# Optimization experiments

Hardware: AMD Instinct MI355X
Metric: run time of the kernel (lower is better)

The kernel has to match this reference:

```python
import jax, jax.numpy as jnp
import numpy as np

BS, H, S, DK = 4, 16, 1024, 64  # bs, n_heads, seq_len(=q_len), head_dim


def setup_inputs() -> dict:
    key = jax.random.key(0)
    k1, k2, k3, k4 = jax.random.split(key, 4)
    return {
        "q": jax.random.normal(k1, (BS, H, S, DK), dtype=jnp.float32),
        "k": jax.random.normal(k2, (BS, H, DK, S), dtype=jnp.float32),
        "v": jax.random.normal(k3, (BS, H, S, DK), dtype=jnp.float32),
        "prev": jax.random.normal(k4, (BS, H, S, S), dtype=jnp.float32),
        "attn_mask": jnp.zeros((1, S, S), dtype=jnp.float32),  # additive float mask
        "key_padding_mask": jnp.zeros((BS, S), dtype=bool),     # True = masked key
        "scale": jnp.asarray(DK ** -0.5, dtype=jnp.float32),    # learnable (lsa=True)
    }


def reference(q, k, v, prev, attn_mask, key_padding_mask, scale):
    # attn_scores = q @ k * scale + prev + attn_mask (float branch)
    scores = jnp.einsum("bhqd,bhdk->bhqk", q, k) * scale
    scores = scores + prev + attn_mask[:, None, :, :]  # [1,S,S] -> broadcast over b,h
    # key_padding_mask: [bs, seq_len] -> masked_fill(-inf)
    scores = jnp.where(key_padding_mask[:, None, None, :], -jnp.inf, scores)
    attn = jax.nn.softmax(scores, axis=-1)  # dropout p=0.0 -> identity
    out = jnp.einsum("bhqk,bhkd->bhqd", attn, v)
    # res_attention=True -> (output, attn_weights, attn_scores)
    return out, attn, scores
```

## Files before the change

### kernel.cpp

```cpp
#include <hip/hip_runtime.h>
#include <math.h>

#define SEQ 1024
#define DKH 64
#define QBLK 64
#define NTILE 16
#define KSTR 68

typedef short s8v __attribute__((ext_vector_type(8)));
typedef short s4v __attribute__((ext_vector_type(4)));
typedef float f4v __attribute__((ext_vector_type(4)));

__device__ __forceinline__ short f2bf(float f) {
    unsigned u = __builtin_bit_cast(unsigned, f);
    return (short)((u + 0x8000u) >> 16);
}
__device__ __forceinline__ s8v ld_frag(const unsigned short* p) {
    s4v a = *(const s4v*)(p);
    s4v b = *(const s4v*)(p + 4);
    s8v r;
    r[0]=a[0]; r[1]=a[1]; r[2]=a[2]; r[3]=a[3];
    r[4]=b[0]; r[5]=b[1]; r[6]=b[2]; r[7]=b[3];
    return r;
}

__global__ __launch_bounds__(256, 3)
void qk_scores(const float* __restrict__ q, const float* __restrict__ k,
               const float* __restrict__ prev, const float* __restrict__ mask,
               const unsigned char* __restrict__ kpm, const float* __restrict__ scale_p,
               float* __restrict__ scores, float* __restrict__ inv_ws)
{
    __shared__ unsigned short q_s[QBLK * KSTR];
    __shared__ unsigned short k_s[64 * KSTR];

    const int t   = threadIdx.x;
    const int w   = t >> 6;
    const int l   = t & 63;
    const int g   = l >> 4;
    const int c16 = l & 15;
    const int sa  = t & 15, sg = t >> 4;

    const int wg  = blockIdx.x;
    const int swz = (wg & 7) * 128 + (wg >> 3);
    const int bh  = swz >> 4;
    const int rt  = swz & 15;
    const int b   = bh >> 4;

    const float scale = *scale_p;

    const float* qb = q    + ((size_t)bh * SEQ + rt * QBLK) * DKH;
    const float* kb = k    + (size_t)bh * DKH * SEQ;
    const float* pb = prev + ((size_t)bh * SEQ + rt * QBLK) * SEQ;
    const float* mb = mask + (size_t)(rt * QBLK) * SEQ;
    const unsigned char* kp = kpm + (size_t)b * SEQ;
    float* sb = scores + ((size_t)bh * SEQ + rt * QBLK) * SEQ;

    {
        const int row = t >> 2, c0 = (t & 3) * 16;
        const float* src = qb + row * DKH + c0;
        #pragma unroll
        for (int j = 0; j < 4; ++j) {
            f4v f = *(const f4v*)(src + 4 * j);
            s4v h; h[0]=f2bf(f[0]); h[1]=f2bf(f[1]); h[2]=f2bf(f[2]); h[3]=f2bf(f[3]);
            *(s4v*)&q_s[row * KSTR + c0 + 4 * j] = h;
        }
    }
    __syncthreads();
    const s8v aq0 = ld_frag(&q_s[(w * 16 + c16) * KSTR + g * 8]);
    const s8v aq1 = ld_frag(&q_s[(w * 16 + c16) * KSTR + 32 + g * 8]);

    f4v kreg[4];
    auto load_K = [&](int ct) {
        const float* src = kb + (size_t)(4 * sg) * SEQ + ct * 64 + 4 * sa;
        kreg[0] = *(const f4v*)(src);
        kreg[1] = *(const f4v*)(src + SEQ);
        kreg[2] = *(const f4v*)(src + 2 * SEQ);
        kreg[3] = *(const f4v*)(src + 3 * SEQ);
    };
    auto load_PM = [&](int ct, float (&pr)[16], float (&mr)[16], int (&kf)[4]) {
        #pragma unroll
        for (int r = 0; r < 4; ++r) {
            const float* prow = pb + (size_t)(w * 16 + 4 * g + r) * SEQ + ct * 64 + c16;
            const float* mrow = mb + (size_t)(w * 16 + 4 * g + r) * SEQ + ct * 64 + c16;
            #pragma unroll
            for (int s = 0; s < 4; ++s) {
                pr[r * 4 + s] = __builtin_nontemporal_load(prow + s * 16);
                mr[r * 4 + s] = mrow[s * 16];
            }
        }
        #pragma unroll
        for (int s = 0; s < 4; ++s) kf[s] = kp[ct * 64 + s * 16 + c16];
    };

    float l_r[4] = {0.f, 0.f, 0.f, 0.f};
    float prA[16], mrA[16], prB[16], mrB[16];
    int kfA[4], kfB[4];
    load_K(0);
    load_PM(0, prA, mrA, kfA);

    auto tile = [&](int ct, float (&prc)[16], float (&mrc)[16], int (&kfc)[4],
                    float (&prn)[16], float (&mrn)[16], int (&kfn)[4]) {
        __syncthreads();
        #pragma unroll
        for (int j = 0; j < 4; ++j) {
            s4v hk; hk[0]=f2bf(kreg[0][j]); hk[1]=f2bf(kreg[1][j]); hk[2]=f2bf(kreg[2][j]); hk[3]=f2bf(kreg[3][j]);
            *(s4v*)&k_s[(4 * sa + j) * KSTR + 4 * sg] = hk;
        }
        __syncthreads();

        if (ct + 1 < NTILE) load_K(ct + 1);

        f4v acc[4];
        #pragma unroll
        for (int s = 0; s < 4; ++s) acc[s] = 0;
        #pragma unroll
        for (int s = 0; s < 4; ++s) {
            const s8v bk0 = ld_frag(&k_s[(s * 16 + c16) * KSTR + g * 8]);
            acc[s] = __builtin_amdgcn_mfma_f32_16x16x32_bf16(aq0, bk0, acc[s], 0, 0, 0);
            const s8v bk1 = ld_frag(&k_s[(s * 16 + c16) * KSTR + 32 + g * 8]);
            acc[s] = __builtin_amdgcn_mfma_f32_16x16x32_bf16(aq1, bk1, acc[s], 0, 0, 0);
        }

        if (ct + 1 < NTILE) load_PM(ct + 1, prn, mrn, kfn);

        const int colb = ct * 64;
        #pragma unroll
        for (int r = 0; r < 4; ++r) {
            float* srow = sb + (size_t)(w * 16 + 4 * g + r) * SEQ + colb + c16;
            #pragma unroll
            for (int s = 0; s < 4; ++s) {
                float x = fmaf(acc[s][r], scale, prc[r * 4 + s] + mrc[r * 4 + s]);
                x = kfc[s] ? -INFINITY : x;
                srow[s * 16] = x;
                l_r[r] += __expf(x);
            }
        }
    };

    for (int c2 = 0; c2 < NTILE; c2 += 2) {
        tile(c2,     prA, mrA, kfA, prB, mrB, kfB);
        tile(c2 + 1, prB, mrB, kfB, prA, mrA, kfA);
    }

    #pragma unroll
    for (int off = 1; off <= 8; off <<= 1) {
        #pragma unroll
        for (int r = 0; r < 4; ++r) l_r[r] += __shfl_xor(l_r[r], off, 64);
    }
    if (c16 == 0) {
        #pragma unroll
        for (int r = 0; r < 4; ++r)
            inv_ws[(size_t)bh * SEQ + rt * QBLK + w * 16 + 4 * g + r] = 1.0f / l_r[r];
    }
}

__global__ __launch_bounds__(256, 3)
void pv_attn(const float* __restrict__ v, const float* __restrict__ scores,
             const float* __restrict__ inv_ws,
             float* __restrict__ attn, float* __restrict__ out)
{
    __shared__ unsigned short v_s[64 * KSTR];
    __shared__ unsigned short e_s[4][16 * KSTR];

    const int t   = threadIdx.x;
    const int w   = t >> 6;
    const int l   = t & 63;
    const int g   = l >> 4;
    const int c16 = l & 15;
    const int sa  = t & 15, sg = t >> 4;

    const int wg  = blockIdx.x;
    const int swz = (wg & 7) * 128 + (wg >> 3);
    const int bh  = swz >> 4;
    const int rt  = swz & 15;

    const float* vb  = v      + (size_t)bh * SEQ * DKH;
    const float* sbr = scores + ((size_t)bh * SEQ + rt * QBLK) * SEQ;
    float* ab = attn + ((size_t)bh * SEQ + rt * QBLK) * SEQ;
    float* ob = out  + ((size_t)bh * SEQ + rt * QBLK) * DKH;

    float inv_r[4];
    #pragma unroll
    for (int r = 0; r < 4; ++r)
        inv_r[r] = inv_ws[(size_t)bh * SEQ + rt * QBLK + w * 16 + g * 4 + r];

    f4v vreg[4];
    auto load_V = [&](int ct) {
        const float* src = vb + (size_t)(ct * 64 + 4 * sg) * DKH + 4 * sa;
        vreg[0] = *(const f4v*)(src);
        vreg[1] = *(const f4v*)(src + DKH);
        vreg[2] = *(const f4v*)(src + 2 * DKH);
        vreg[3] = *(const f4v*)(src + 3 * DKH);
    };
    auto load_S = [&](int ct, f4v (&sr)[4]) {
        #pragma unroll
        for (int r = 0; r < 4; ++r)
            sr[r] = *(const f4v*)(sbr + (size_t)(w * 16 + g * 4 + r) * SEQ + ct * 64 + c16 * 4);
    };

    f4v oacc[4];
    #pragma unroll
    for (int d = 0; d < 4; ++d) oacc[d] = 0;

    f4v sregA[4], sregB[4];
    load_V(0);
    load_S(0, sregA);

    auto tile = [&](int ct, f4v (&sc)[4], f4v (&sn)[4]) {
        __syncthreads();
        #pragma unroll
        for (int j = 0; j < 4; ++j) {
            s4v hv; hv[0]=f2bf(vreg[0][j]); hv[1]=f2bf(vreg[1][j]); hv[2]=f2bf(vreg[2][j]); hv[3]=f2bf(vreg[3][j]);
            *(s4v*)&v_s[(4 * sa + j) * KSTR + 4 * sg] = hv;
        }
        __syncthreads();

        if (ct + 1 < NTILE) { load_V(ct + 1); load_S(ct + 1, sn); }

        #pragma unroll
        for (int r = 0; r < 4; ++r) {
            const f4v s4 = sc[r];
            const float e0 = __expf(s4[0]);
            const float e1 = __expf(s4[1]);
            const float e2 = __expf(s4[2]);
            const float e3 = __expf(s4[3]);
            f4v aw; aw[0]=e0*inv_r[r]; aw[1]=e1*inv_r[r]; aw[2]=e2*inv_r[r]; aw[3]=e3*inv_r[r];
            __builtin_nontemporal_store(aw,
                (f4v*)(ab + (size_t)(w * 16 + g * 4 + r) * SEQ + ct * 64 + c16 * 4));
            s4v h; h[0]=f2bf(e0); h[1]=f2bf(e1); h[2]=f2bf(e2); h[3]=f2bf(e3);
            *(s4v*)&e_s[w][(g * 4 + r) * KSTR + c16 * 4] = h;
        }

        #pragma unroll
        for (int ks = 0; ks < 2; ++ks) {
            const s8v ae = ld_frag(&e_s[w][c16 * KSTR + ks * 32 + g * 8]);
            #pragma unroll
            for (int d = 0; d < 4; ++d) {
                const s8v bv = ld_frag(&v_s[(d * 16 + c16) * KSTR + ks * 32 + g * 8]);
                oacc[d] = __builtin_amdgcn_mfma_f32_16x16x32_bf16(ae, bv, oacc[d], 0, 0, 0);
            }
        }
    };

    for (int c2 = 0; c2 < NTILE; c2 += 2) {
        tile(c2,     sregA, sregB);
        tile(c2 + 1, sregB, sregA);
    }

    #pragma unroll
    for (int d = 0; d < 4; ++d) {
        #pragma unroll
        for (int r = 0; r < 4; ++r)
            __builtin_nontemporal_store(oacc[d][r] * inv_r[r],
                ob + (size_t)(w * 16 + g * 4 + r) * DKH + d * 16 + c16);
    }
}

extern "C" void kernel_launch(void* const* d_in, const int* in_sizes, int n_in,
                              void* d_out, int out_size, void* d_ws, size_t ws_size,
                              hipStream_t stream) {
    const float* q    = (const float*)d_in[0];
    const float* k    = (const float*)d_in[1];
    const float* v    = (const float*)d_in[2];
    const float* prev = (const float*)d_in[3];
    const float* mask = (const float*)d_in[4];
    const unsigned char* kpm = (const unsigned char*)d_in[5];
    const float* scale = (const float*)d_in[6];

    float* out    = (float*)d_out;
    float* attn   = out  + (size_t)4 * 16 * SEQ * DKH;
    float* scores = attn + (size_t)4 * 16 * SEQ * SEQ;
    float* inv_ws = (float*)d_ws;

    qk_scores<<<dim3(1024), dim3(256), 0, stream>>>(q, k, prev, mask, kpm, scale,
                                                    scores, inv_ws);
    pv_attn<<<dim3(1024), dim3(256), 0, stream>>>(v, scores, inv_ws, attn, out);
}
```

Before: 276.9 us.

## Fuse score and PV kernels into one kernel re-reading scores within block

```diff
diff --git a/kernel.cpp b/kernel.cpp
--- a/kernel.cpp
+++ b/kernel.cpp
@@ -24,14 +24,18 @@
     return r;
 }
 
-__global__ __launch_bounds__(256, 3)
-void qk_scores(const float* __restrict__ q, const float* __restrict__ k,
-               const float* __restrict__ prev, const float* __restrict__ mask,
-               const unsigned char* __restrict__ kpm, const float* __restrict__ scale_p,
-               float* __restrict__ scores, float* __restrict__ inv_ws)
+__global__ __launch_bounds__(256, 4)
+void attn_fused(const float* __restrict__ q, const float* __restrict__ k,
+                const float* __restrict__ v, const float* __restrict__ prev,
+                const float* __restrict__ mask, const unsigned char* __restrict__ kpm,
+                const float* __restrict__ scale_p,
+                float* __restrict__ out, float* __restrict__ attn,
+                float* __restrict__ scores)
 {
     __shared__ unsigned short q_s[QBLK * KSTR];
-    __shared__ unsigned short k_s[64 * KSTR];
+    __shared__ unsigned short kv_s[64 * KSTR];
+    __shared__ unsigned short e_s[4][16 * KSTR];
+    __shared__ float inv_sh[QBLK];
 
     const int t   = threadIdx.x;
     const int w   = t >> 6;
@@ -50,10 +54,13 @@
 
     const float* qb = q    + ((size_t)bh * SEQ + rt * QBLK) * DKH;
     const float* kb = k    + (size_t)bh * DKH * SEQ;
+    const float* vb = v    + (size_t)bh * SEQ * DKH;
     const float* pb = prev + ((size_t)bh * SEQ + rt * QBLK) * SEQ;
     const float* mb = mask + (size_t)(rt * QBLK) * SEQ;
     const unsigned char* kp = kpm + (size_t)b * SEQ;
     float* sb = scores + ((size_t)bh * SEQ + rt * QBLK) * SEQ;
+    float* ab = attn   + ((size_t)bh * SEQ + rt * QBLK) * SEQ;
+    float* ob = out    + ((size_t)bh * SEQ + rt * QBLK) * DKH;
 
     {
         const int row = t >> 2, c0 = (t & 3) * 16;
@@ -77,34 +84,28 @@
         kreg[2] = *(const f4v*)(src + 2 * SEQ);
         kreg[3] = *(const f4v*)(src + 3 * SEQ);
     };
-    auto load_PM = [&](int ct, float (&pr)[16], float (&mr)[16], int (&kf)[4]) {
+    auto load_PM = [&](int ct, float (&pm)[16]) {
         #pragma unroll
         for (int r = 0; r < 4; ++r) {
             const float* prow = pb + (size_t)(w * 16 + 4 * g + r) * SEQ + ct * 64 + c16;
             const float* mrow = mb + (size_t)(w * 16 + 4 * g + r) * SEQ + ct * 64 + c16;
             #pragma unroll
-            for (int s = 0; s < 4; ++s) {
-                pr[r * 4 + s] = __builtin_nontemporal_load(prow + s * 16);
-                mr[r * 4 + s] = mrow[s * 16];
-            }
-        }
-        #pragma unroll
-        for (int s = 0; s < 4; ++s) kf[s] = kp[ct * 64 + s * 16 + c16];
+            for (int s = 0; s < 4; ++s)
+                pm[r * 4 + s] = __builtin_nontemporal_load(prow + s * 16) + mrow[s * 16];
+        }
     };
 
     float l_r[4] = {0.f, 0.f, 0.f, 0.f};
-    float prA[16], mrA[16], prB[16], mrB[16];
-    int kfA[4], kfB[4];
+    float pmA[16], pmB[16];
     load_K(0);
-    load_PM(0, prA, mrA, kfA);
-
-    auto tile = [&](int ct, float (&prc)[16], float (&mrc)[16], int (&kfc)[4],
-                    float (&prn)[16], float (&mrn)[16], int (&kfn)[4]) {
+    load_PM(0, pmA);
+
+    auto tile1 = [&](int ct, float (&pmc)[16], float (&pmn)[16]) {
         __syncthreads();
         #pragma unroll
         for (int j = 0; j < 4; ++j) {
             s4v hk; hk[0]=f2bf(kreg[0][j]); hk[1]=f2bf(kreg[1][j]); hk[2]=f2bf(kreg[2][j]); hk[3]=f2bf(kreg[3][j]);
-            *(s4v*)&k_s[(4 * sa + j) * KSTR + 4 * sg] = hk;
+            *(s4v*)&kv_s[(4 * sa + j) * KSTR + 4 * sg] = hk;
         }
         __syncthreads();
 
@@ -115,22 +116,25 @@
         for (int s = 0; s < 4; ++s) acc[s] = 0;
         #pragma unroll
         for (int s = 0; s < 4; ++s) {
-            const s8v bk0 = ld_frag(&k_s[(s * 16 + c16) * KSTR + g * 8]);
+            const s8v bk0 = ld_frag(&kv_s[(s * 16 + c16) * KSTR + g * 8]);
             acc[s] = __builtin_amdgcn_mfma_f32_16x16x32_bf16(aq0, bk0, acc[s], 0, 0, 0);
-            const s8v bk1 = ld_frag(&k_s[(s * 16 + c16) * KSTR + 32 + g * 8]);
+            const s8v bk1 = ld_frag(&kv_s[(s * 16 + c16) * KSTR + 32 + g * 8]);
             acc[s] = __builtin_amdgcn_mfma_f32_16x16x32_bf16(aq1, bk1, acc[s], 0, 0, 0);
         }
 
-        if (ct + 1 < NTILE) load_PM(ct + 1, prn, mrn, kfn);
+        if (ct + 1 < NTILE) load_PM(ct + 1, pmn);
 
         const int colb = ct * 64;
+        int kf[4];
+        #pragma unroll
+        for (int s = 0; s < 4; ++s) kf[s] = kp[colb + s * 16 + c16];
         #pragma unroll
         for (int r = 0; r < 4; ++r) {
             float* srow = sb + (size_t)(w * 16 + 4 * g + r) * SEQ + colb + c16;
             #pragma unroll
             for (int s = 0; s < 4; ++s) {
-                float x = fmaf(acc[s][r], scale, prc[r * 4 + s] + mrc[r * 4 + s]);
-                x = kfc[s] ? -INFINITY : x;
+                float x = fmaf(acc[s][r], scale, pmc[r * 4 + s]);
+                x = kf[s] ? -INFINITY : x;
                 srow[s * 16] = x;
                 l_r[r] += __expf(x);
             }
@@ -138,8 +142,8 @@
     };
 
     for (int c2 = 0; c2 < NTILE; c2 += 2) {
-        tile(c2,     prA, mrA, kfA, prB, mrB, kfB);
-        tile(c2 + 1, prB, mrB, kfB, prA, mrA, kfA);
+        tile1(c2,     pmA, pmB);
+        tile1(c2 + 1, pmB, pmA);
     }
 
     #pragma unroll
@@ -147,42 +151,17 @@
         #pragma unroll
         for (int r = 0; r < 4; ++r) l_r[r] += __shfl_xor(l_r[r], off, 64);
     }
+    float inv_r[4];
+    #pragma unroll
+    for (int r = 0; r < 4; ++r) inv_r[r] = 1.0f / l_r[r];
     if (c16 == 0) {
         #pragma unroll
-        for (int r = 0; r < 4; ++r)
-            inv_ws[(size_t)bh * SEQ + rt * QBLK + w * 16 + 4 * g + r] = 1.0f / l_r[r];
-    }
-}
-
-__global__ __launch_bounds__(256, 3)
-void pv_attn(const float* __restrict__ v, const float* __restrict__ scores,
-             const float* __restrict__ inv_ws,
-             float* __restrict__ attn, float* __restrict__ out)
-{
-    __shared__ unsigned short v_s[64 * KSTR];
-    __shared__ unsigned short e_s[4][16 * KSTR];
-
-    const int t   = threadIdx.x;
-    const int w   = t >> 6;
-    const int l   = t & 63;
-    const int g   = l >> 4;
-    const int c16 = l & 15;
-    const int sa  = t & 15, sg = t >> 4;
-
-    const int wg  = blockIdx.x;
-    const int swz = (wg & 7) * 128 + (wg >> 3);
-    const int bh  = swz >> 4;
-    const int rt  = swz & 15;
-
-    const float* vb  = v      + (size_t)bh * SEQ * DKH;
-    const float* sbr = scores + ((size_t)bh * SEQ + rt * QBLK) * SEQ;
-    float* ab = attn + ((size_t)bh * SEQ + rt * QBLK) * SEQ;
-    float* ob = out  + ((size_t)bh * SEQ + rt * QBLK) * DKH;
-
-    float inv_r[4];
-    #pragma unroll
-    for (int r = 0; r < 4; ++r)
-        inv_r[r] = inv_ws[(size_t)bh * SEQ + rt * QBLK + w * 16 + g * 4 + r];
+        for (int r = 0; r < 4; ++r) inv_sh[w * 16 + 4 * g + r] = inv_r[r];
+    }
+
+    const int lr = l >> 2, cq = l & 3;
+    __syncthreads();
+    const float inv_use = inv_sh[w * 16 + lr];
 
     f4v vreg[4];
     auto load_V = [&](int ct) {
@@ -192,43 +171,43 @@
         vreg[2] = *(const f4v*)(src + 2 * DKH);
         vreg[3] = *(const f4v*)(src + 3 * DKH);
     };
-    auto load_S = [&](int ct, f4v (&sr)[4]) {
-        #pragma unroll
-        for (int r = 0; r < 4; ++r)
-            sr[r] = *(const f4v*)(sbr + (size_t)(w * 16 + g * 4 + r) * SEQ + ct * 64 + c16 * 4);
-    };
 
     f4v oacc[4];
     #pragma unroll
     for (int d = 0; d < 4; ++d) oacc[d] = 0;
 
     f4v sregA[4], sregB[4];
+    auto load_Srow = [&](int ct, f4v (&sr)[4]) {
+        #pragma unroll
+        for (int j = 0; j < 4; ++j)
+            sr[j] = *(const f4v*)(sb + (size_t)(w * 16 + lr) * SEQ + ct * 64 + cq * 16 + 4 * j);
+    };
     load_V(0);
-    load_S(0, sregA);
-
-    auto tile = [&](int ct, f4v (&sc)[4], f4v (&sn)[4]) {
+    load_Srow(0, sregA);
+
+    auto tile2 = [&](int ct, f4v (&sc)[4], f4v (&sn)[4]) {
         __syncthreads();
         #pragma unroll
         for (int j = 0; j < 4; ++j) {
             s4v hv; hv[0]=f2bf(vreg[0][j]); hv[1]=f2bf(vreg[1][j]); hv[2]=f2bf(vreg[2][j]); hv[3]=f2bf(vreg[3][j]);
-            *(s4v*)&v_s[(4 * sa + j) * KSTR + 4 * sg] = hv;
-        }
-        __syncthreads();
-
-        if (ct + 1 < NTILE) { load_V(ct + 1); load_S(ct + 1, sn); }
-
-        #pragma unroll
-        for (int r = 0; r < 4; ++r) {
-            const f4v s4 = sc[r];
+            *(s4v*)&kv_s[(4 * sa + j) * KSTR + 4 * sg] = hv;
+        }
+        __syncthreads();
+
+        if (ct + 1 < NTILE) { load_V(ct + 1); load_Srow(ct + 1, sn); }
+
+        #pragma unroll
+        for (int j = 0; j < 4; ++j) {
+            const f4v s4 = sc[j];
             const float e0 = __expf(s4[0]);
             const float e1 = __expf(s4[1]);
             const float e2 = __expf(s4[2]);
             const float e3 = __expf(s4[3]);
-            f4v aw; aw[0]=e0*inv_r[r]; aw[1]=e1*inv_r[r]; aw[2]=e2*inv_r[r]; aw[3]=e3*inv_r[r];
+            f4v aw; aw[0]=e0*inv_use; aw[1]=e1*inv_use; aw[2]=e2*inv_use; aw[3]=e3*inv_use;
             __builtin_nontemporal_store(aw,
-                (f4v*)(ab + (size_t)(w * 16 + g * 4 + r) * SEQ + ct * 64 + c16 * 4));
+                (f4v*)(ab + (size_t)(w * 16 + lr) * SEQ + ct * 64 + cq * 16 + 4 * j));
             s4v h; h[0]=f2bf(e0); h[1]=f2bf(e1); h[2]=f2bf(e2); h[3]=f2bf(e3);
-            *(s4v*)&e_s[w][(g * 4 + r) * KSTR + c16 * 4] = h;
+            *(s4v*)&e_s[w][lr * KSTR + cq * 16 + 4 * j] = h;
         }
 
         #pragma unroll
@@ -236,15 +215,15 @@
             const s8v ae = ld_frag(&e_s[w][c16 * KSTR + ks * 32 + g * 8]);
             #pragma unroll
             for (int d = 0; d < 4; ++d) {
-                const s8v bv = ld_frag(&v_s[(d * 16 + c16) * KSTR + ks * 32 + g * 8]);
+                const s8v bv = ld_frag(&kv_s[(d * 16 + c16) * KSTR + ks * 32 + g * 8]);
                 oacc[d] = __builtin_amdgcn_mfma_f32_16x16x32_bf16(ae, bv, oacc[d], 0, 0, 0);
             }
         }
     };
 
     for (int c2 = 0; c2 < NTILE; c2 += 2) {
-        tile(c2,     sregA, sregB);
-        tile(c2 + 1, sregB, sregA);
+        tile2(c2,     sregA, sregB);
+        tile2(c2 + 1, sregB, sregA);
     }
 
     #pragma unroll
@@ -252,7 +231,7 @@
         #pragma unroll
         for (int r = 0; r < 4; ++r)
             __builtin_nontemporal_store(oacc[d][r] * inv_r[r],
-                ob + (size_t)(w * 16 + g * 4 + r) * DKH + d * 16 + c16);
+                ob + (size_t)(w * 16 + 4 * g + r) * DKH + d * 16 + c16);
     }
 }
 
@@ -270,9 +249,7 @@
     float* out    = (float*)d_out;
     float* attn   = out  + (size_t)4 * 16 * SEQ * DKH;
     float* scores = attn + (size_t)4 * 16 * SEQ * SEQ;
-    float* inv_ws = (float*)d_ws;
-
-    qk_scores<<<dim3(1024), dim3(256), 0, stream>>>(q, k, prev, mask, kpm, scale,
-                                                    scores, inv_ws);
-    pv_attn<<<dim3(1024), dim3(256), 0, stream>>>(v, scores, inv_ws, attn, out);
-}
+
+    attn_fused<<<dim3(1024), dim3(256), 0, stream>>>(q, k, v, prev, mask, kpm, scale,
+                                                     out, attn, scores);
+}
```

New measurement: 680.1 us. 2.46x slower.
